# Optimization experiments

Hardware: AMD Instinct MI355X
Metric: run time of the kernel (lower is better)

## Reference

```python
import jax, jax.numpy as jnp
import numpy as np


def setup_inputs() -> dict:
    key = jax.random.key(0)
    B, C, W, H = 32, 256, 56, 56
    G, GS = 64, 4  # 64 channel groups of size 4 (covers all 256 channels)
    x = jax.random.normal(key, (B, C, W, H), dtype=jnp.float32)
    cols = jnp.arange(G * GS, dtype=jnp.int32).reshape(G, GS)
    return {"x": x, "cols": cols}


def reference(x, cols):
    # StaticCGM: within each channel group, keep only the max channel per
    # (batch, spatial) position, zero the others, then ReLU.
    B, C, W, H = x.shape
    G, GS = cols.shape
    xg = x[:, cols]  # [B, G, GS, W, H] gather of grouped channels
    idx = jnp.argmax(xg, axis=2)  # [B, G, W, H] winning member per group
    mask = idx[:, :, None] == jnp.arange(GS, dtype=idx.dtype)[None, None, :, None, None]
    masked = jnp.where(mask, xg, jnp.zeros((), dtype=x.dtype))  # zero non-winners
    # Scatter grouped result back to original channel positions.
    out = jnp.zeros_like(x).at[:, cols.reshape(-1)].set(
        masked.reshape(B, G * GS, W, H)
    )
    return jax.nn.relu(out)
```

## Files before the change

kernel.cpp:

```cpp
#include <hip/hip_runtime.h>

constexpr int B  = 32;
constexpr int C  = 256;
constexpr int P  = 56 * 56;
constexpr int G  = 64;
constexpr int GS = 4;
constexpr int F  = P / 4;
constexpr int TOTAL4 = B * G * F;
constexpr int BLOCK = 256;
constexpr int PER_THREAD = 2;
constexpr int BLOCKS = TOTAL4 / (BLOCK * PER_THREAD);

typedef float fx4 __attribute__((ext_vector_type(4)));

__global__ __launch_bounds__(BLOCK) void cgm_kernel(const float* __restrict__ x,
                                                    const int* __restrict__ cols,
                                                    float* __restrict__ out) {
    int t  = threadIdx.x;
    int k0 = blockIdx.x * (BLOCK * PER_THREAD) + t;

    long off[PER_THREAD][GS];
#pragma unroll
    for (int i = 0; i < PER_THREAD; ++i) {
        int k  = k0 + i * BLOCK;
        int u  = k % F;
        int bg = k / F;
        int g  = bg & (G - 1);
        int b  = bg >> 6;
#pragma unroll
        for (int s = 0; s < GS; ++s) {
            int c = cols[g * GS + s];
            off[i][s] = ((long)b * C + c) * P + (long)u * 4;
        }
    }

    fx4 v[PER_THREAD][GS];
#pragma unroll
    for (int i = 0; i < PER_THREAD; ++i)
#pragma unroll
        for (int s = 0; s < GS; ++s)
            v[i][s] = *reinterpret_cast<const fx4*>(x + off[i][s]);

    __builtin_amdgcn_sched_barrier(0);

#pragma unroll
    for (int i = 0; i < PER_THREAD; ++i) {
        fx4 o[GS];
#pragma unroll
        for (int s = 0; s < GS; ++s) o[s] = (fx4)0.0f;

#pragma unroll
        for (int j = 0; j < 4; ++j) {
            int   bi   = 0;
            float best = v[i][0][j];
#pragma unroll
            for (int s = 1; s < GS; ++s) {
                if (v[i][s][j] > best) { best = v[i][s][j]; bi = s; }
            }
            float r = best > 0.0f ? best : 0.0f;
#pragma unroll
            for (int s = 0; s < GS; ++s) {
                if (s == bi) o[s][j] = r;
            }
        }

#pragma unroll
        for (int s = 0; s < GS; ++s)
            *reinterpret_cast<fx4*>(out + off[i][s]) = o[s];
    }
}

extern "C" void kernel_launch(void* const* d_in, const int* in_sizes, int n_in,
                              void* d_out, int out_size, void* d_ws, size_t ws_size,
                              hipStream_t stream) {
    const float* x    = (const float*)d_in[0];
    const int*   cols = (const int*)d_in[1];
    float*       out  = (float*)d_out;

    cgm_kernel<<<dim3(BLOCKS), dim3(BLOCK), 0, stream>>>(x, cols, out);
}
```

Measured before the change: 181.3 us.

## Loop each thread over batch strides with software-prefetched double-buffered loads

Each thread now handles 8 positions spaced a batch stride apart (4 batches each) instead of 2 adjacent ones, so the grid is 4x smaller. Index math and the cols lookups are done once per thread, and the next iteration's four vector loads are issued before the current iteration's compute and stores. The aim is to overlap memory latency with work and amortise setup, at the cost of fewer resident waves and less memory-level parallelism per wave than issuing all loads up front.

```diff
diff --git a/kernel.cpp b/kernel.cpp
--- a/kernel.cpp
+++ b/kernel.cpp
@@ -7,55 +7,54 @@
 constexpr int GS = 4;
 constexpr int F  = P / 4;
 constexpr int TOTAL4 = B * G * F;
-constexpr int BLOCK = 256;
-constexpr int PER_THREAD = 2;
-constexpr int BLOCKS = TOTAL4 / (BLOCK * PER_THREAD);
+constexpr int BLOCK  = 256;
+constexpr int ITERS  = 8;
+constexpr int GRIDTH = TOTAL4 / ITERS;
+constexpr int BLOCKS = GRIDTH / BLOCK;
 
 typedef float fx4 __attribute__((ext_vector_type(4)));
 
 __global__ __launch_bounds__(BLOCK) void cgm_kernel(const float* __restrict__ x,
                                                     const int* __restrict__ cols,
                                                     float* __restrict__ out) {
-    int t  = threadIdx.x;
-    int k0 = blockIdx.x * (BLOCK * PER_THREAD) + t;
+    int k0 = blockIdx.x * BLOCK + threadIdx.x;
 
-    long off[PER_THREAD][GS];
+    int u  = k0 % F;
+    int bg = k0 / F;
+    int g  = bg & (G - 1);
+    int b0 = bg >> 6;
+
+    long off[GS];
 #pragma unroll
-    for (int i = 0; i < PER_THREAD; ++i) {
-        int k  = k0 + i * BLOCK;
-        int u  = k % F;
-        int bg = k / F;
-        int g  = bg & (G - 1);
-        int b  = bg >> 6;
+    for (int s = 0; s < GS; ++s) {
+        int c = cols[g * GS + s];
+        off[s] = ((long)b0 * C + c) * (long)P + (long)u * 4;
+    }
+    const long DELTA = (long)(B / ITERS) * C * P;
+
+    fx4 cur[GS], nxt[GS];
 #pragma unroll
-        for (int s = 0; s < GS; ++s) {
-            int c = cols[g * GS + s];
-            off[i][s] = ((long)b * C + c) * P + (long)u * 4;
-        }
-    }
-
-    fx4 v[PER_THREAD][GS];
-#pragma unroll
-    for (int i = 0; i < PER_THREAD; ++i)
-#pragma unroll
-        for (int s = 0; s < GS; ++s)
-            v[i][s] = *reinterpret_cast<const fx4*>(x + off[i][s]);
-
-    __builtin_amdgcn_sched_barrier(0);
+    for (int s = 0; s < GS; ++s)
+        cur[s] = *reinterpret_cast<const fx4*>(x + off[s]);
 
 #pragma unroll
-    for (int i = 0; i < PER_THREAD; ++i) {
+    for (int i = 0; i < ITERS; ++i) {
+        if (i + 1 < ITERS) {
+#pragma unroll
+            for (int s = 0; s < GS; ++s)
+                nxt[s] = *reinterpret_cast<const fx4*>(x + off[s] + DELTA);
+        }
+
         fx4 o[GS];
 #pragma unroll
         for (int s = 0; s < GS; ++s) o[s] = (fx4)0.0f;
-
 #pragma unroll
         for (int j = 0; j < 4; ++j) {
             int   bi   = 0;
-            float best = v[i][0][j];
+            float best = cur[0][j];
 #pragma unroll
             for (int s = 1; s < GS; ++s) {
-                if (v[i][s][j] > best) { best = v[i][s][j]; bi = s; }
+                if (cur[s][j] > best) { best = cur[s][j]; bi = s; }
             }
             float r = best > 0.0f ? best : 0.0f;
 #pragma unroll
@@ -66,7 +65,13 @@
 
 #pragma unroll
         for (int s = 0; s < GS; ++s)
-            *reinterpret_cast<fx4*>(out + off[i][s]) = o[s];
+            *reinterpret_cast<fx4*>(out + off[s]) = o[s];
+
+#pragma unroll
+        for (int s = 0; s < GS; ++s) {
+            off[s] += DELTA;
+            cur[s] = nxt[s];
+        }
     }
 }
 
```

Measured after the change: 184.6 us. About the same (+1.8%).

## Stage each (batch, group) channel block through LDS with one block per group

Applied to the files above, without the earlier changes.

Changes the decomposition so each workgroup handles one (batch, group) pair. It first copies all four channels' spatial planes into 50KB of shared memory, then synchronises and computes the argmax mask from LDS. The goal is more contiguous streaming loads per channel plane and less per-element index math. In exchange it adds an LDS round trip and a block barrier, and the large LDS footprint limits occupancy.

```diff
diff --git a/kernel.cpp b/kernel.cpp
--- a/kernel.cpp
+++ b/kernel.cpp
@@ -6,67 +6,73 @@
 constexpr int G  = 64;
 constexpr int GS = 4;
 constexpr int F  = P / 4;
-constexpr int TOTAL4 = B * G * F;
 constexpr int BLOCK = 256;
-constexpr int PER_THREAD = 2;
-constexpr int BLOCKS = TOTAL4 / (BLOCK * PER_THREAD);
+constexpr int BLOCKS = B * G;
 
 typedef float fx4 __attribute__((ext_vector_type(4)));
 
 __global__ __launch_bounds__(BLOCK) void cgm_kernel(const float* __restrict__ x,
                                                     const int* __restrict__ cols,
                                                     float* __restrict__ out) {
-    int t  = threadIdx.x;
-    int k0 = blockIdx.x * (BLOCK * PER_THREAD) + t;
+    __shared__ float lds[GS * P];
 
-    long off[PER_THREAD][GS];
+    int t = threadIdx.x;
+    int g = blockIdx.x & (G - 1);
+    int b = blockIdx.x >> 6;
+
+    long base[GS];
 #pragma unroll
-    for (int i = 0; i < PER_THREAD; ++i) {
-        int k  = k0 + i * BLOCK;
-        int u  = k % F;
-        int bg = k / F;
-        int g  = bg & (G - 1);
-        int b  = bg >> 6;
+    for (int s = 0; s < GS; ++s) {
+        int c = cols[g * GS + s];
+        base[s] = ((long)b * C + c) * (long)P;
+    }
+
 #pragma unroll
-        for (int s = 0; s < GS; ++s) {
-            int c = cols[g * GS + s];
-            off[i][s] = ((long)b * C + c) * P + (long)u * 4;
+    for (int s = 0; s < GS; ++s) {
+#pragma unroll
+        for (int i = 0; i < 4; ++i) {
+            int u4 = i * BLOCK + t;
+            if (u4 < F) {
+                fx4 v = *reinterpret_cast<const fx4*>(x + base[s] + (long)u4 * 4);
+                *reinterpret_cast<fx4*>(&lds[s * P + u4 * 4]) = v;
+            }
         }
     }
 
-    fx4 v[PER_THREAD][GS];
-#pragma unroll
-    for (int i = 0; i < PER_THREAD; ++i)
-#pragma unroll
-        for (int s = 0; s < GS; ++s)
-            v[i][s] = *reinterpret_cast<const fx4*>(x + off[i][s]);
-
-    __builtin_amdgcn_sched_barrier(0);
+    __syncthreads();
 
 #pragma unroll
-    for (int i = 0; i < PER_THREAD; ++i) {
-        fx4 o[GS];
+    for (int i = 0; i < 4; ++i) {
+        int u4 = i * BLOCK + t;
+        if (u4 < F) {
+            fx4 v[GS];
 #pragma unroll
-        for (int s = 0; s < GS; ++s) o[s] = (fx4)0.0f;
+            for (int s = 0; s < GS; ++s)
+                v[s] = *reinterpret_cast<const fx4*>(&lds[s * P + u4 * 4]);
+
+            fx4 o[GS];
+#pragma unroll
+            for (int s = 0; s < GS; ++s) o[s] = (fx4)0.0f;
 
 #pragma unroll
-        for (int j = 0; j < 4; ++j) {
-            int   bi   = 0;
-            float best = v[i][0][j];
+            for (int j = 0; j < 4; ++j) {
+                int   bi   = 0;
+                float best = v[0][j];
 #pragma unroll
-            for (int s = 1; s < GS; ++s) {
-                if (v[i][s][j] > best) { best = v[i][s][j]; bi = s; }
+                for (int s = 1; s < GS; ++s) {
+                    if (v[s][j] > best) { best = v[s][j]; bi = s; }
+                }
+                float r = best > 0.0f ? best : 0.0f;
+#pragma unroll
+                for (int s = 0; s < GS; ++s) {
+                    if (s == bi) o[s][j] = r;
+                }
             }
-            float r = best > 0.0f ? best : 0.0f;
-#pragma unroll
-            for (int s = 0; s < GS; ++s) {
-                if (s == bi) o[s][j] = r;
-            }
-        }
 
 #pragma unroll
-        for (int s = 0; s < GS; ++s)
-            *reinterpret_cast<fx4*>(out + off[i][s]) = o[s];
+            for (int s = 0; s < GS; ++s)
+                *reinterpret_cast<fx4*>(out + base[s] + (long)u4 * 4) = o[s];
+        }
     }
 }
 
```

Result: slower. 186.9 us (+3.1%).
